# Kernel tuning notes

Hardware: AMD Instinct MI355X
Metric: run time of the kernel (lower is better)

The kernel has to match this reference:

```python
import jax, jax.numpy as jnp
import numpy as np

B, D, KM1 = 8192, 256, 64  # batch, feature dim (no bias), num_classes-1
NC = KM1 + 1


def setup_inputs() -> dict:
    key = jax.random.key(0)
    k1, k2, k3 = jax.random.split(key, 3)
    features = jax.random.normal(k1, (B, D), dtype=jnp.float32)
    y = jax.random.randint(k2, (B,), 0, NC)
    mu = jax.random.normal(k3, (D, KM1), dtype=jnp.float32) * 0.001
    Sigma = jnp.broadcast_to(jnp.eye(D, dtype=jnp.float32), (KM1, D, D)).copy()
    return {"features": features, "y": y, "mu": mu, "Sigma": Sigma, "loss_type": 1}


def _b_ky(nc):
    # (nc, nc-1) stick-breaking selector matrix
    return 1.0 - jnp.pad(jnp.eye(nc)[..., :-2], [(0, 0), (1, 0)]).cumsum(-1)


def reference(features, y, mu, Sigma, loss_type):
    x = features                      # use_bias=False -> pad is a no-op
    logits = x @ mu                   # (B, K-1)
    bky = _b_ky(NC)                   # (K, K-1)
    y1h = jax.nn.one_hot(y, NC)       # (B, K)
    if loss_type == 0:
        full = jnp.pad(logits, [(0, 0), (0, 1)]) - jax.nn.softplus(logits) @ bky.T
        return -jnp.sum(full * y1h, -1)
    else:
        # psi_k = sqrt(x^T (Sigma_k + mu_k mu_k^T) x) = sqrt(x^T Sigma_k x + (x.mu_k)^2)
        xSx = jnp.einsum('bd,kde,be->bk', x, Sigma, x)   # (B, K-1)
        psi = jnp.sqrt(xSx + logits * logits)
        b = y1h @ bky                 # (B, K-1)
        kappa = y1h[..., :-1] - b / 2
        return -jnp.sum(logits * kappa + b * (psi / 2 - jax.nn.softplus(psi)), -1)
```

## Files before the change

### kernel.cpp

```cpp
#include <hip/hip_runtime.h>

typedef __attribute__((ext_vector_type(8))) short bf16x8;
typedef __attribute__((ext_vector_type(4))) float f32x4;

#define B_N 8192
#define D_N 256
#define K_N 64

__device__ __forceinline__ unsigned short bf16_rne(float f) {
  unsigned u = __builtin_bit_cast(unsigned, f);
  u += 0x7fffu + ((u >> 16) & 1u);
  return (unsigned short)(u >> 16);
}
__device__ __forceinline__ float bf16_f32(unsigned short h) {
  return __builtin_bit_cast(float, (unsigned)h << 16);
}

__device__ __forceinline__ void gload_lds16(const void* g, void* l) {
  __builtin_amdgcn_global_load_lds(
      (const __attribute__((address_space(1))) unsigned int*)g,
      (__attribute__((address_space(3))) unsigned int*)l, 16, 0, 0);
}

__global__ void convert_kernel(const float* __restrict__ src,
                               ushort* __restrict__ hi, ushort* __restrict__ lo,
                               int n4) {
  int idx = blockIdx.x * blockDim.x + threadIdx.x;
  int stride = gridDim.x * blockDim.x;
  for (int i = idx; i < n4; i += stride) {
    float4 v = ((const float4*)src)[i];
    ushort4 h, l;
    h.x = bf16_rne(v.x); l.x = bf16_rne(v.x - bf16_f32(h.x));
    h.y = bf16_rne(v.y); l.y = bf16_rne(v.y - bf16_f32(h.y));
    h.z = bf16_rne(v.z); l.z = bf16_rne(v.z - bf16_f32(h.z));
    h.w = bf16_rne(v.w); l.w = bf16_rne(v.w - bf16_f32(h.w));
    ((ushort4*)hi)[i] = h;
    ((ushort4*)lo)[i] = l;
  }
}

__global__ void convert_T_kernel(const float* __restrict__ Sigma,
                                 ushort* __restrict__ Th,
                                 ushort* __restrict__ Tl) {
  const int dtab[10] = {0, 0, 0, 0, 1, 1, 1, 2, 2, 3};
  const int etab[10] = {0, 1, 2, 3, 1, 2, 3, 2, 3, 3};
  const int k = blockIdx.x;
  const int dblk = dtab[blockIdx.y], eblk = etab[blockIdx.y];
  const float wgt = (dblk == eblk) ? 0.5f : 1.0f;
  const int tid = threadIdx.x;
  const int dl = tid >> 2;
  const int el0 = (tid & 3) * 16;
  const int d = dblk * 64 + dl;
  const size_t rowbase = ((size_t)k * D_N + d) * D_N + eblk * 64 + el0;
  const float* Srow = Sigma + rowbase;
  const float* Scol = Sigma + ((size_t)k * D_N + eblk * 64 + el0) * D_N + d;
  ushort h[16], l[16];
#pragma unroll
  for (int i = 0; i < 16; ++i) {
    const float t = (Srow[i] + Scol[(size_t)i * D_N]) * wgt;
    h[i] = bf16_rne(t);
    l[i] = bf16_rne(t - bf16_f32(h[i]));
  }
  *(uint4*)(Th + rowbase) = *(uint4*)&h[0];
  *(uint4*)(Th + rowbase + 8) = *(uint4*)&h[8];
  *(uint4*)(Tl + rowbase) = *(uint4*)&l[0];
  *(uint4*)(Tl + rowbase + 8) = *(uint4*)&l[8];
}

__global__ __launch_bounds__(256, 4) void xsx_tri3_kernel(
    const float* __restrict__ X,
    const ushort* __restrict__ Xh, const ushort* __restrict__ Xl,
    const ushort* __restrict__ Th, const ushort* __restrict__ Tl,
    float* __restrict__ part) {
  __shared__ __align__(16) ushort A_h[128][32];
  __shared__ __align__(16) ushort A_l[128][32];
  __shared__ __align__(16) ushort B_h[64][32];
  __shared__ __align__(16) ushort B_l[64][32];

  const int tid = threadIdx.x;
  const int lane = tid & 63;
  const int wid = tid >> 6;
  const int lr = lane & 15;
  const int lk = lane >> 4;

  const int bid = blockIdx.x;
  const int xcd = bid & 7;
  const int r = bid >> 3;
  const int qd = r >> 9;
  const int s = r & 511;
  const int kk = xcd * 8 + (s & 7);
  const int bg = s >> 3;
  const int bbase = bg * 128;

  const int srow = lane >> 2;
  const int sc = ((lane & 3) ^ ((lane >> 3) & 3)) * 8;
  const int rdc = (lk ^ ((lr >> 1) & 3)) * 8;

  f32x4 acc[2][4];
#pragma unroll
  for (int mi = 0; mi < 2; ++mi)
#pragma unroll
    for (int ni = 0; ni < 4; ++ni) acc[mi][ni] = (f32x4){0.f, 0.f, 0.f, 0.f};

  const size_t a0 = (size_t)(bbase + wid * 32 + srow) * D_N + sc;
  const size_t bK = (size_t)kk * (D_N * D_N) +
                    (size_t)(qd * 64 + wid * 16 + srow) * D_N + sc;

  const int nch = 2 * (4 - qd);
  for (int c = 0; c < nch; ++c) {
    const int e0 = qd * 64 + c * 32;
    __syncthreads();
    gload_lds16(Xh + a0 + e0, &A_h[wid * 32][0]);
    gload_lds16(Xh + a0 + (size_t)16 * D_N + e0, &A_h[wid * 32 + 16][0]);
    gload_lds16(Xl + a0 + e0, &A_l[wid * 32][0]);
    gload_lds16(Xl + a0 + (size_t)16 * D_N + e0, &A_l[wid * 32 + 16][0]);
    gload_lds16(Th + bK + e0, &B_h[wid * 16][0]);
    gload_lds16(Tl + bK + e0, &B_l[wid * 16][0]);
    __syncthreads();

    bf16x8 ah[2], al[2];
#pragma unroll
    for (int mi = 0; mi < 2; ++mi) {
      ah[mi] = *(const bf16x8*)&A_h[wid * 32 + mi * 16 + lr][rdc];
      al[mi] = *(const bf16x8*)&A_l[wid * 32 + mi * 16 + lr][rdc];
    }
#pragma unroll
    for (int ni = 0; ni < 4; ++ni) {
      const bf16x8 bh = *(const bf16x8*)&B_h[ni * 16 + lr][rdc];
      const bf16x8 bl = *(const bf16x8*)&B_l[ni * 16 + lr][rdc];
#pragma unroll
      for (int mi = 0; mi < 2; ++mi)
        acc[mi][ni] = __builtin_amdgcn_mfma_f32_16x16x32_bf16(
            ah[mi], bh, acc[mi][ni], 0, 0, 0);
#pragma unroll
      for (int mi = 0; mi < 2; ++mi)
        acc[mi][ni] = __builtin_amdgcn_mfma_f32_16x16x32_bf16(
            al[mi], bh, acc[mi][ni], 0, 0, 0);
#pragma unroll
      for (int mi = 0; mi < 2; ++mi)
        acc[mi][ni] = __builtin_amdgcn_mfma_f32_16x16x32_bf16(
            ah[mi], bl, acc[mi][ni], 0, 0, 0);
    }
  }

#pragma unroll
  for (int mi = 0; mi < 2; ++mi) {
#pragma unroll
    for (int jj = 0; jj < 4; ++jj) {
      const int brow = bbase + wid * 32 + mi * 16 + lk * 4 + jj;
      const float* xr = X + (size_t)brow * D_N + qd * 64 + lr;
      float p = 0.f;
#pragma unroll
      for (int ni = 0; ni < 4; ++ni) p = fmaf(acc[mi][ni][jj], xr[ni * 16], p);
      p += __shfl_xor(p, 1);
      p += __shfl_xor(p, 2);
      p += __shfl_xor(p, 4);
      p += __shfl_xor(p, 8);
      if (lr == 0) part[((size_t)brow * K_N + kk) * 4 + qd] = p;
    }
  }
}

__global__ __launch_bounds__(512, 2) void xsx_fallback(
    const float* __restrict__ X, const float* __restrict__ Sigma,
    float* __restrict__ xsx) {
  constexpr int BM = 128, KT = 32;
  __shared__ __align__(16) ushort Ah[BM][KT];
  __shared__ __align__(16) ushort Al[BM][KT];
  __shared__ __align__(16) ushort Bh[D_N][KT];
  __shared__ __align__(16) ushort Bl[D_N][KT];
  __shared__ float red[4][BM];

  const int tid = threadIdx.x;
  const int lane = tid & 63;
  const int wid = tid >> 6;
  const int wm = wid >> 2;
  const int wn = wid & 3;
  const int lr = lane & 15;
  const int lk = lane >> 4;

  const int b0 = blockIdx.x * BM;
  const int kk = blockIdx.y;
  const size_t soff = (size_t)kk * D_N * D_N;

  f32x4 acc[4][4];
#pragma unroll
  for (int mi = 0; mi < 4; ++mi)
#pragma unroll
    for (int ni = 0; ni < 4; ++ni) acc[mi][ni] = (f32x4){0.f, 0.f, 0.f, 0.f};

  for (int ec = 0; ec < D_N / KT; ++ec) {
    const int e0 = ec * KT;
    __syncthreads();
#pragma unroll
    for (int r = 0; r < 2; ++r) {
      const int i = tid + 512 * r;
      const int row = i >> 3, c4 = (i & 7) * 4;
      const float4 v = *(const float4*)(X + (size_t)(b0 + row) * D_N + e0 + c4);
      ushort4 h, l;
      h.x = bf16_rne(v.x); l.x = bf16_rne(v.x - bf16_f32(h.x));
      h.y = bf16_rne(v.y); l.y = bf16_rne(v.y - bf16_f32(h.y));
      h.z = bf16_rne(v.z); l.z = bf16_rne(v.z - bf16_f32(h.z));
      h.w = bf16_rne(v.w); l.w = bf16_rne(v.w - bf16_f32(h.w));
      *(ushort4*)&Ah[row][c4] = h;
      *(ushort4*)&Al[row][c4] = l;
    }
#pragma unroll
    for (int r = 0; r < 4; ++r) {
      const int i = tid + 512 * r;
      const int d = i >> 3, c4 = (i & 7) * 4;
      const float4 v = *(const float4*)(Sigma + soff + (size_t)d * D_N + e0 + c4);
      ushort4 h, l;
      h.x = bf16_rne(v.x); l.x = bf16_rne(v.x - bf16_f32(h.x));
      h.y = bf16_rne(v.y); l.y = bf16_rne(v.y - bf16_f32(h.y));
      h.z = bf16_rne(v.z); l.z = bf16_rne(v.z - bf16_f32(h.z));
      h.w = bf16_rne(v.w); l.w = bf16_rne(v.w - bf16_f32(h.w));
      *(ushort4*)&Bh[d][c4] = h;
      *(ushort4*)&Bl[d][c4] = l;
    }
    __syncthreads();

    bf16x8 ah[4], al[4];
#pragma unroll
    for (int mi = 0; mi < 4; ++mi) {
      ah[mi] = *(const bf16x8*)&Ah[wm * 64 + mi * 16 + lr][lk * 8];
      al[mi] = *(const bf16x8*)&Al[wm * 64 + mi * 16 + lr][lk * 8];
    }
#pragma unroll
    for (int ni = 0; ni < 4; ++ni) {
      const bf16x8 bh = *(const bf16x8*)&Bh[wn * 64 + ni * 16 + lr][lk * 8];
      const bf16x8 bl = *(const bf16x8*)&Bl[wn * 64 + ni * 16 + lr][lk * 8];
#pragma unroll
      for (int mi = 0; mi < 4; ++mi) {
        acc[mi][ni] = __builtin_amdgcn_mfma_f32_16x16x32_bf16(ah[mi], bh, acc[mi][ni], 0, 0, 0);
        acc[mi][ni] = __builtin_amdgcn_mfma_f32_16x16x32_bf16(al[mi], bh, acc[mi][ni], 0, 0, 0);
        acc[mi][ni] = __builtin_amdgcn_mfma_f32_16x16x32_bf16(ah[mi], bl, acc[mi][ni], 0, 0, 0);
      }
    }
  }

  float p[4][4];
#pragma unroll
  for (int mi = 0; mi < 4; ++mi)
#pragma unroll
    for (int jj = 0; jj < 4; ++jj) p[mi][jj] = 0.f;
#pragma unroll
  for (int mi = 0; mi < 4; ++mi) {
#pragma unroll
    for (int jj = 0; jj < 4; ++jj) {
      const int brow = b0 + wm * 64 + mi * 16 + lk * 4 + jj;
      const float* xr = X + (size_t)brow * D_N + wn * 64 + lr;
#pragma unroll
      for (int ni = 0; ni < 4; ++ni)
        p[mi][jj] = fmaf(acc[mi][ni][jj], xr[ni * 16], p[mi][jj]);
    }
  }
#pragma unroll
  for (int mi = 0; mi < 4; ++mi)
#pragma unroll
    for (int jj = 0; jj < 4; ++jj) {
      float v = p[mi][jj];
      v += __shfl_xor(v, 1);
      v += __shfl_xor(v, 2);
      v += __shfl_xor(v, 4);
      v += __shfl_xor(v, 8);
      p[mi][jj] = v;
    }
  if (lr == 0) {
#pragma unroll
    for (int mi = 0; mi < 4; ++mi)
#pragma unroll
      for (int jj = 0; jj < 4; ++jj)
        red[wn][wm * 64 + mi * 16 + lk * 4 + jj] = p[mi][jj];
  }
  __syncthreads();
  if (tid < BM) {
    const float s = red[0][tid] + red[1][tid] + red[2][tid] + red[3][tid];
    xsx[(size_t)(b0 + tid) * K_N + kk] = s;
  }
}

__global__ __launch_bounds__(256) void loss_kernel2(
    const float* __restrict__ X, const int* __restrict__ y,
    const float* __restrict__ mu, const int* __restrict__ loss_type,
    const float* __restrict__ xsx, float* __restrict__ out, int nparts) {
  __shared__ float mu_s[D_N * K_N];
  __shared__ float x_s[32][D_N];
  const int tid = threadIdx.x;
  const int wid = tid >> 6;
  const int lane = tid & 63;
  const int brow0 = blockIdx.x * 32;

  for (int i = tid; i < D_N * K_N / 4; i += 256)
    ((float4*)mu_s)[i] = ((const float4*)mu)[i];
#pragma unroll
  for (int i = 0; i < 8; ++i) {
    const int row = (tid >> 6) * 8 + i;
    ((float4*)&x_s[row][0])[lane] =
        ((const float4*)(X + (size_t)(brow0 + row) * D_N))[lane];
  }
  __syncthreads();

  const int lt = loss_type[0];

  for (int i = 0; i < 8; ++i) {
    const int row = wid * 8 + i;
    const int b = brow0 + row;
    const int yb = y[b];

    float logit = 0.f;
#pragma unroll 8
    for (int d = 0; d < D_N; ++d)
      logit = fmaf(x_s[row][d], mu_s[d * K_N + lane], logit);

    float term;
    if (lt == 1) {
      float xv;
      if (nparts == 4) {
        const float4 pv = *(const float4*)(xsx + ((size_t)b * K_N + lane) * 4);
        xv = ((pv.x + pv.y) + pv.z) + pv.w;
      } else {
        xv = xsx[(size_t)b * K_N + lane];
      }
      const float psi = sqrtf(fmaxf(xv + logit * logit, 0.f));
      const float bk = (lane <= yb) ? 1.f : 0.f;
      const float kap = ((lane == yb) ? 1.f : 0.f) - 0.5f * bk;
      term = logit * kap + bk * (-0.5f * psi - log1pf(expf(-psi)));
    } else {
      const float sp = (logit > 0.f) ? (logit + log1pf(expf(-logit)))
                                     : log1pf(expf(logit));
      term = ((lane == yb) ? logit : 0.f) - ((lane <= yb) ? sp : 0.f);
    }
#pragma unroll
    for (int s = 1; s < 64; s <<= 1) term += __shfl_xor(term, s);
    if (lane == 0) out[b] = -term;
  }
}

extern "C" void kernel_launch(void* const* d_in, const int* in_sizes, int n_in,
                              void* d_out, int out_size, void* d_ws, size_t ws_size,
                              hipStream_t stream) {
  const float* X = (const float*)d_in[0];
  const int* y = (const int*)d_in[1];
  const float* mu = (const float*)d_in[2];
  const float* Sigma = (const float*)d_in[3];
  const int* lt = (const int*)d_in[4];
  float* out = (float*)d_out;

  const size_t XN = (size_t)B_N * D_N;
  const size_t SN = (size_t)K_N * D_N * D_N;
  const size_t xh_off = 0;
  const size_t xl_off = xh_off + XN * 2;
  const size_t th_off = xl_off + XN * 2;
  const size_t tl_off = th_off + SN * 2;
  const size_t part_off = tl_off + SN * 2;
  const size_t need = part_off + (size_t)B_N * K_N * 4 * 4;

  char* w = (char*)d_ws;
  if (ws_size >= need) {
    ushort* Xh = (ushort*)(w + xh_off);
    ushort* Xl = (ushort*)(w + xl_off);
    ushort* Th = (ushort*)(w + th_off);
    ushort* Tl = (ushort*)(w + tl_off);
    float* part = (float*)(w + part_off);
    hipLaunchKernelGGL(convert_kernel, dim3(1024), dim3(256), 0, stream,
                       X, Xh, Xl, (int)(XN / 4));
    hipLaunchKernelGGL(convert_T_kernel, dim3(64, 10), dim3(256), 0, stream,
                       Sigma, Th, Tl);
    hipLaunchKernelGGL(xsx_tri3_kernel, dim3(16384), dim3(256), 0, stream,
                       X, Xh, Xl, Th, Tl, part);
    hipLaunchKernelGGL(loss_kernel2, dim3(B_N / 32), dim3(256), 0, stream,
                       X, y, mu, lt, part, out, 4);
  } else {
    float* xsx = (float*)w;
    hipLaunchKernelGGL(xsx_fallback, dim3(B_N / 128, K_N), dim3(512), 0, stream,
                       X, Sigma, xsx);
    hipLaunchKernelGGL(loss_kernel2, dim3(B_N / 32), dim3(256), 0, stream,
                       X, y, mu, lt, xsx, out, 1);
  }
}
```

Measured before the change: 200.4 us.

## Double-buffer Sigma tiles in LDS and load X fragments directly to registers

Restructures the xSx MFMA kernel main loop into a two-stage software pipeline. The Sigma hi/lo tiles are double-buffered in LDS, and the X hi/lo fragments now go straight from global memory into registers, no longer through LDS. The aim is to overlap the next chunk's loads with the current chunk's MFMAs and to drop one sync plus the A-side LDS traffic. In exchange it needs more registers for the prefetched fragments and relies on uncoalesced 16-byte direct global reads of X, which could hurt under the 4-wave occupancy bound.

```diff
diff --git a/kernel.cpp b/kernel.cpp
--- a/kernel.cpp
+++ b/kernel.cpp
@@ -67,15 +67,12 @@
   *(uint4*)(Tl + rowbase + 8) = *(uint4*)&l[8];
 }
 
-__global__ __launch_bounds__(256, 4) void xsx_tri3_kernel(
+__global__ __launch_bounds__(256, 4) void xsx_tri4_kernel(
     const float* __restrict__ X,
     const ushort* __restrict__ Xh, const ushort* __restrict__ Xl,
     const ushort* __restrict__ Th, const ushort* __restrict__ Tl,
     float* __restrict__ part) {
-  __shared__ __align__(16) ushort A_h[128][32];
-  __shared__ __align__(16) ushort A_l[128][32];
-  __shared__ __align__(16) ushort B_h[64][32];
-  __shared__ __align__(16) ushort B_l[64][32];
+  __shared__ __align__(16) ushort Bb[2][2][64 * 32];
 
   const int tid = threadIdx.x;
   const int lane = tid & 63;
@@ -102,32 +99,26 @@
 #pragma unroll
     for (int ni = 0; ni < 4; ++ni) acc[mi][ni] = (f32x4){0.f, 0.f, 0.f, 0.f};
 
-  const size_t a0 = (size_t)(bbase + wid * 32 + srow) * D_N + sc;
+  const size_t aA = (size_t)(bbase + wid * 32 + lr) * D_N + lk * 8;
   const size_t bK = (size_t)kk * (D_N * D_N) +
                     (size_t)(qd * 64 + wid * 16 + srow) * D_N + sc;
 
-  const int nch = 2 * (4 - qd);
-  for (int c = 0; c < nch; ++c) {
-    const int e0 = qd * 64 + c * 32;
-    __syncthreads();
-    gload_lds16(Xh + a0 + e0, &A_h[wid * 32][0]);
-    gload_lds16(Xh + a0 + (size_t)16 * D_N + e0, &A_h[wid * 32 + 16][0]);
-    gload_lds16(Xl + a0 + e0, &A_l[wid * 32][0]);
-    gload_lds16(Xl + a0 + (size_t)16 * D_N + e0, &A_l[wid * 32 + 16][0]);
-    gload_lds16(Th + bK + e0, &B_h[wid * 16][0]);
-    gload_lds16(Tl + bK + e0, &B_l[wid * 16][0]);
-    __syncthreads();
-
-    bf16x8 ah[2], al[2];
+  auto loadA = [&](bf16x8(&dh)[2], bf16x8(&dl)[2], int E) {
 #pragma unroll
     for (int mi = 0; mi < 2; ++mi) {
-      ah[mi] = *(const bf16x8*)&A_h[wid * 32 + mi * 16 + lr][rdc];
-      al[mi] = *(const bf16x8*)&A_l[wid * 32 + mi * 16 + lr][rdc];
-    }
+      dh[mi] = *(const bf16x8*)(Xh + aA + (size_t)(mi * 16) * D_N + E);
+      dl[mi] = *(const bf16x8*)(Xl + aA + (size_t)(mi * 16) * D_N + E);
+    }
+  };
+  auto stageB = [&](int buf, int E) {
+    gload_lds16(Th + bK + E, &Bb[buf][0][wid * 16 * 32]);
+    gload_lds16(Tl + bK + E, &Bb[buf][1][wid * 16 * 32]);
+  };
+  auto compute = [&](const bf16x8(&ah)[2], const bf16x8(&al)[2], int buf) {
 #pragma unroll
     for (int ni = 0; ni < 4; ++ni) {
-      const bf16x8 bh = *(const bf16x8*)&B_h[ni * 16 + lr][rdc];
-      const bf16x8 bl = *(const bf16x8*)&B_l[ni * 16 + lr][rdc];
+      const bf16x8 bh = *(const bf16x8*)&Bb[buf][0][(ni * 16 + lr) * 32 + rdc];
+      const bf16x8 bl = *(const bf16x8*)&Bb[buf][1][(ni * 16 + lr) * 32 + rdc];
 #pragma unroll
       for (int mi = 0; mi < 2; ++mi)
         acc[mi][ni] = __builtin_amdgcn_mfma_f32_16x16x32_bf16(
@@ -141,6 +132,28 @@
         acc[mi][ni] = __builtin_amdgcn_mfma_f32_16x16x32_bf16(
             ah[mi], bl, acc[mi][ni], 0, 0, 0);
     }
+  };
+
+  const int nch = 2 * (4 - qd);
+  bf16x8 a0h[2], a0l[2], a1h[2], a1l[2];
+
+  loadA(a0h, a0l, qd * 64);
+  stageB(0, qd * 64);
+  __syncthreads();
+
+  for (int c = 0; c < nch; c += 2) {
+    const int e1 = qd * 64 + (c + 1) * 32;
+    loadA(a1h, a1l, e1);
+    stageB(1, e1);
+    compute(a0h, a0l, 0);
+    __syncthreads();
+    if (c + 2 < nch) {
+      const int e2 = qd * 64 + (c + 2) * 32;
+      loadA(a0h, a0l, e2);
+      stageB(0, e2);
+    }
+    compute(a1h, a1l, 1);
+    __syncthreads();
   }
 
 #pragma unroll
@@ -367,7 +380,7 @@
                        X, Xh, Xl, (int)(XN / 4));
     hipLaunchKernelGGL(convert_T_kernel, dim3(64, 10), dim3(256), 0, stream,
                        Sigma, Th, Tl);
-    hipLaunchKernelGGL(xsx_tri3_kernel, dim3(16384), dim3(256), 0, stream,
+    hipLaunchKernelGGL(xsx_tri4_kernel, dim3(16384), dim3(256), 0, stream,
                        X, Xh, Xl, Th, Tl, part);
     hipLaunchKernelGGL(loss_kernel2, dim3(B_N / 32), dim3(256), 0, stream,
                        X, y, mu, lt, part, out, 4);
```

Result: slower. 253.0 us (+26.3%).
